# Performance work log

Hardware: AMD Instinct MI355X
Metric: run time of the kernel (lower is better)

## Reference

```python
import jax, jax.numpy as jnp
import numpy as np

D_MODEL = 512
NHEAD = 8
HEAD_DIM = D_MODEL // NHEAD


def setup_inputs() -> dict:
    key = jax.random.key(0)
    ks = jax.random.split(key, 12)
    B, T = 2, 4096
    inp = {
        'query': jax.random.normal(ks[0], (B, T, D_MODEL), jnp.float32),
        'key': jax.random.normal(ks[1], (B, T, D_MODEL), jnp.float32),
        'value': jax.random.normal(ks[2], (B, T, D_MODEL), jnp.float32),
        'frac': jax.random.uniform(ks[3], (B, T), jnp.float32),
        # learned parameters (torch nn.Linear: y = x @ W.T + b)
        'Wq': jax.random.normal(ks[4], (D_MODEL, D_MODEL), jnp.float32) * (D_MODEL ** -0.5),
        'bq': jnp.zeros((D_MODEL,), jnp.float32),
        'Wk': jax.random.normal(ks[5], (D_MODEL, D_MODEL), jnp.float32) * (D_MODEL ** -0.5),
        'bk': jnp.zeros((D_MODEL,), jnp.float32),
        'Wv': jax.random.normal(ks[6], (D_MODEL, D_MODEL), jnp.float32) * (D_MODEL ** -0.5),
        'bv': jnp.zeros((D_MODEL,), jnp.float32),
        'Wo': jax.random.normal(ks[7], (D_MODEL, D_MODEL), jnp.float32) * (D_MODEL ** -0.5),
        'bo': jnp.zeros((D_MODEL,), jnp.float32),
        'alpha_pos': jax.random.normal(ks[8], (NHEAD,), jnp.float32) * 0.1,
        'alpha_neg': jax.random.normal(ks[9], (NHEAD,), jnp.float32) * 0.1,
    }
    return inp


def reference(query, key, value, frac, Wq, bq, Wk, bk, Wv, bv, Wo, bo, alpha_pos, alpha_neg):
    B, T, _ = query.shape
    scale = HEAD_DIM ** -0.5
    # projections (torch Linear convention: x @ W.T + b)
    Q = (query @ Wq.T + bq).reshape(B, T, NHEAD, HEAD_DIM).transpose(0, 2, 1, 3)
    K = (key @ Wk.T + bk).reshape(B, T, NHEAD, HEAD_DIM).transpose(0, 2, 1, 3)
    V = (value @ Wv.T + bv).reshape(B, T, NHEAD, HEAD_DIM).transpose(0, 2, 1, 3)
    scores = jnp.einsum('bhqd,bhkd->bhqk', Q, K) * scale  # [B,H,T,T]
    # stoichiometric bias: D[b,i,j] = frac[b,j] - frac[b,i]
    D = frac[:, None, :] - frac[:, :, None]  # [B,T,T]
    D_pos = jnp.maximum(D, 0.0)
    D_neg = jnp.minimum(D, 0.0)
    bias = (alpha_pos[None, :, None, None] * D_pos[:, None]
            + alpha_neg[None, :, None, None] * D_neg[:, None])  # [B,H,T,T]
    probs = jax.nn.softmax(scores + bias, axis=-1)
    out = jnp.einsum('bhqk,bhkd->bhqd', probs, V)
    out = out.transpose(0, 2, 1, 3).reshape(B, T, D_MODEL)
    return out @ Wo.T + bo
```

## Files before the change

kernel.cpp:

```cpp
#include <hip/hip_runtime.h>

typedef __attribute__((ext_vector_type(8))) __bf16 bf16x8;
typedef __attribute__((ext_vector_type(8))) unsigned short ushort8;
typedef __attribute__((ext_vector_type(4))) unsigned short ushort4_t;
typedef __attribute__((ext_vector_type(4))) float f32x4;
typedef unsigned short ushort_t;

#define MFMA_BF16(A,B,C) __builtin_amdgcn_mfma_f32_16x16x32_bf16(A,B,C,0,0,0)

#define T_SEQ 4096
#define DM 512
#define HD_ 64
#define NH_ 8

#define LOG2E 1.4426950408889634f
#define QSCALE (0.125f * LOG2E)

__device__ __forceinline__ unsigned short f2b(float f){
    unsigned int u = __builtin_bit_cast(unsigned int, f);
    u += 0x7FFFu + ((u >> 16) & 1u);
    return (unsigned short)(u >> 16);
}

__device__ __forceinline__ float exp2_fast(float x){
#if __has_builtin(__builtin_amdgcn_exp2f)
    return __builtin_amdgcn_exp2f(x);
#else
    float r; asm("v_exp_f32 %0, %1" : "=v"(r) : "v"(x)); return r;
#endif
}

__device__ __forceinline__ float max3f(float a, float b, float c){
    return fmaxf(fmaxf(a, b), c);
}

__device__ __forceinline__ unsigned cvt_pk_bf16(float a, float b){
    unsigned r;
    asm("v_cvt_pk_bf16_f32 %0, %1, %2" : "=v"(r) : "v"(a), "v"(b));
    return r;
}

__device__ __forceinline__ void gload_lds16(const void* g, void* l){
    __builtin_amdgcn_global_load_lds((const __attribute__((address_space(1))) void*)g,
                                     (__attribute__((address_space(3))) void*)l, 16, 0, 0);
}

template<int MODE>
__device__ __forceinline__ void gemm_body(const float* __restrict__ A, const float* __restrict__ W,
                                          const float* __restrict__ bias, void* __restrict__ Cout,
                                          int m0, int n0, float scale)
{
    constexpr int K = 512, N = 512;
    __shared__ ushort_t As[128*64];
    __shared__ ushort_t Bs[128*64];

    const int tid  = threadIdx.x;
    const int lane = tid & 63;
    const int w    = tid >> 6;
    const int g    = lane >> 4;
    const int c16  = lane & 15;
    const int wm   = w >> 1, wn = w & 1;

    f32x4 acc[4][4];
#pragma unroll
    for (int i=0;i<4;i++)
#pragma unroll
        for (int j=0;j<4;j++) acc[i][j] = (f32x4){0.f,0.f,0.f,0.f};

#pragma unroll 1
    for (int kt=0; kt<K/64; kt++){
        __syncthreads();
#pragma unroll
        for (int j=0;j<4;j++){
            int cid = j*256 + tid;
            int row = cid >> 3, ch = cid & 7;
            const float* srcA = A + (size_t)(m0+row)*K + kt*64 + ch*8;
            const float* srcB = W + (size_t)(n0+row)*K + kt*64 + ch*8;
            float4 a0 = *(const float4*)srcA;
            float4 a1 = *(const float4*)(srcA+4);
            float4 b0 = *(const float4*)srcB;
            float4 b1 = *(const float4*)(srcB+4);
            ushort8 va, vb;
            va[0]=f2b(a0.x); va[1]=f2b(a0.y); va[2]=f2b(a0.z); va[3]=f2b(a0.w);
            va[4]=f2b(a1.x); va[5]=f2b(a1.y); va[6]=f2b(a1.z); va[7]=f2b(a1.w);
            vb[0]=f2b(b0.x); vb[1]=f2b(b0.y); vb[2]=f2b(b0.z); vb[3]=f2b(b0.w);
            vb[4]=f2b(b1.x); vb[5]=f2b(b1.y); vb[6]=f2b(b1.z); vb[7]=f2b(b1.w);
            int dst = row*64 + ((ch ^ (row & 7))<<3);
            *(ushort8*)&As[dst] = va;
            *(ushort8*)&Bs[dst] = vb;
        }
        __syncthreads();
#pragma unroll
        for (int ks=0; ks<2; ks++){
            bf16x8 af[4], bfr[4];
#pragma unroll
            for (int f=0; f<4; f++){
                int rowa = wm*64 + f*16 + c16;
                af[f]  = *(const bf16x8*)&As[rowa*64 + (((ks*4+g) ^ (rowa&7))<<3)];
                int rowb = wn*64 + f*16 + c16;
                bfr[f] = *(const bf16x8*)&Bs[rowb*64 + (((ks*4+g) ^ (rowb&7))<<3)];
            }
#pragma unroll
            for (int fm=0; fm<4; fm++)
#pragma unroll
                for (int fn=0; fn<4; fn++)
                    acc[fm][fn] = MFMA_BF16(af[fm], bfr[fn], acc[fm][fn]);
        }
    }
#pragma unroll
    for (int fm=0; fm<4; fm++)
#pragma unroll
        for (int fn=0; fn<4; fn++){
            int col = n0 + wn*64 + fn*16 + c16;
            float bv = bias[col];
            if (MODE == 2){
                int t0r = m0 + wm*64 + fm*16 + g*4;
                int b2  = t0r >> 12;
                int t   = t0r & 4095;
                int h2  = col >> 6, d = col & 63;
                ushort4_t u;
#pragma unroll
                for (int r=0; r<4; r++) u[r] = f2b(acc[fm][fn][r] + bv);
                ushort_t* dst = (ushort_t*)Cout + ((size_t)(b2*NH_ + h2)*HD_ + d)*T_SEQ + t;
                *(ushort4_t*)dst = u;
            } else {
#pragma unroll
                for (int r=0; r<4; r++){
                    int rowm = m0 + wm*64 + fm*16 + g*4 + r;
                    float vv = (acc[fm][fn][r] + bv) * scale;
                    if (MODE == 1) ((ushort_t*)Cout)[(size_t)rowm*N + col] = f2b(vv);
                    else           ((float*)Cout)[(size_t)rowm*N + col]   = vv;
                }
            }
        }
}

__global__ __launch_bounds__(256,2) void gemm_qkv_kernel(
    const float* __restrict__ q, const float* __restrict__ k, const float* __restrict__ v,
    const float* __restrict__ Wq, const float* __restrict__ bq,
    const float* __restrict__ Wk, const float* __restrict__ bk,
    const float* __restrict__ Wv, const float* __restrict__ bv,
    ushort_t* __restrict__ QKVp)
{
    int z = blockIdx.z;
    const float* A  = (z==0) ? q  : (z==1 ? k  : v);
    const float* W  = (z==0) ? Wq : (z==1 ? Wk : Wv);
    const float* bb = (z==0) ? bq : (z==1 ? bk : bv);
    ushort_t* C = QKVp + (size_t)z * (size_t)(2*T_SEQ) * DM;
    if (z == 2)
        gemm_body<2>(A, W, bb, C, blockIdx.x*128, blockIdx.y*128, 1.0f);
    else
        gemm_body<1>(A, W, bb, C, blockIdx.x*128, blockIdx.y*128,
                     (z==0) ? QSCALE : 1.0f);
}

__global__ __launch_bounds__(256,2) void gemm_out_kernel(
    const float* __restrict__ O, const float* __restrict__ Wo,
    const float* __restrict__ bo, float* __restrict__ out)
{
    gemm_body<0>(O, Wo, bo, out, blockIdx.x*128, blockIdx.y*128, 1.0f);
}

__global__ __launch_bounds__(512,4) void flash_kernel(
    const ushort_t* __restrict__ Qp, const ushort_t* __restrict__ Kp, const ushort_t* __restrict__ Vt,
    const float* __restrict__ frac, const float* __restrict__ alphap, const float* __restrict__ alphan,
    float* __restrict__ O)
{
    int i    = blockIdx.x;
    int slot = i & 7;
    int seq  = i >> 3;
    int bh   = slot*2 + (seq >> 5);
    int qt   = seq & 31;
    int b    = bh >> 3, h = bh & 7;
    int q0   = qt * 128;

    const int tid  = threadIdx.x;
    const int w    = tid >> 6;
    const int lane = tid & 63;
    const int g    = lane >> 4;
    const int c16  = lane & 15;

    __shared__ ushort_t Ks [2][64*64];
    __shared__ ushort_t VTs[2][64*64];
    __shared__ ushort_t PW [8][16*64];

    const ushort_t* Qbase = Qp + (size_t)(b*T_SEQ)*DM + h*HD_;
    const ushort_t* Kbase = Kp + (size_t)(b*T_SEQ)*DM + h*HD_;
    const ushort_t* Vtb   = Vt + (size_t)bh*HD_*T_SEQ;
    const float*    fr    = frac + b*T_SEQ;
    const float c1 = 0.5f*(alphap[h] + alphan[h]) * LOG2E;
    const float c2 = 0.5f*(alphap[h] - alphan[h]) * LOG2E;
    const int qrow = q0 + w*16;

    bf16x8 qa[2];
#pragma unroll
    for (int ks=0; ks<2; ks++)
        qa[ks] = *(const bf16x8*)(Qbase + (size_t)(qrow + c16)*DM + ks*32 + g*8);
    const float fi = fr[qrow + c16];

    ushort8 ou;
#pragma unroll
    for (int j=0;j<8;j++) ou[j] = 0x3F80;
    const bf16x8 ones = __builtin_bit_cast(bf16x8, ou);

    float m2 = -1e30f;
    f32x4 acc[4];
    f32x4 asum;
#pragma unroll
    for (int dt=0; dt<4; dt++) acc[dt] = (f32x4){0.f,0.f,0.f,0.f};
    asum = (f32x4){0.f,0.f,0.f,0.f};

    bf16x8 vbp[2][4];

#define STAGE(BUF, KV0)                                                          \
    {                                                                            \
        int cb  = w*64;                                                          \
        int idx = cb + lane;                                                     \
        int row = idx >> 3, cc = idx & 7;                                        \
        int cs  = cc ^ (row & 7);                                                \
        gload_lds16(Kbase + (size_t)((KV0)+row)*DM + cs*8, &Ks[BUF][cb*8]);      \
        gload_lds16(Vtb + (size_t)row*T_SEQ + (KV0) + cs*8, &VTs[BUF][cb*8]);    \
    }

    STAGE(0, 0);
    asm volatile("s_waitcnt vmcnt(0)" ::: "memory");
    __syncthreads();

    int buf = 0;
#pragma unroll 1
    for (int kt=0; kt<T_SEQ/64; kt++){
        int kv0 = kt*64;
        if (kt+1 < T_SEQ/64) STAGE(buf^1, kv0+64);

        bf16x8 pb0, pb1;
        if (kt > 0){
            pb0 = *(const bf16x8*)&PW[w][c16*64 + (((    g) ^ (c16&7))<<3)];
            pb1 = *(const bf16x8*)&PW[w][c16*64 + (((4 + g) ^ (c16&7))<<3)];
        }

        f32x4 s[4];
#pragma unroll
        for (int n=0; n<4; n++) s[n] = (f32x4){0.f,0.f,0.f,0.f};
        __builtin_amdgcn_s_setprio(1);
#pragma unroll
        for (int n=0; n<4; n++){
#pragma unroll
            for (int ks=0; ks<2; ks++){
                int row = n*16 + c16;
                bf16x8 kb = *(const bf16x8*)&Ks[buf][row*64 + (((ks*4+g) ^ (row&7))<<3)];
                s[n] = MFMA_BF16(kb, qa[ks], s[n]);
            }
        }
        if (kt > 0){
            asum = MFMA_BF16(ones, pb0, asum);
#pragma unroll
            for (int dt=0; dt<4; dt++) acc[dt] = MFMA_BF16(vbp[0][dt], pb0, acc[dt]);
            asum = MFMA_BF16(ones, pb1, asum);
#pragma unroll
            for (int dt=0; dt<4; dt++) acc[dt] = MFMA_BF16(vbp[1][dt], pb1, acc[dt]);
        }
        __builtin_amdgcn_s_setprio(0);
        __builtin_amdgcn_sched_barrier(0);

#pragma unroll
        for (int n=0; n<4; n++){
            f32x4 fj = *(const f32x4*)&fr[kv0 + n*16 + g*4];
#pragma unroll
            for (int r=0; r<4; r++){
                float dd = fj[r] - fi;
                s[n][r] = fmaf(c1, dd, fmaf(c2, fabsf(dd), s[n][r]));
            }
        }
        float mx;
        {
            float t0 = max3f(s[0][0], s[0][1], s[0][2]);
            float t1 = max3f(s[0][3], s[1][0], s[1][1]);
            float t2 = max3f(s[1][2], s[1][3], s[2][0]);
            float t3 = max3f(s[2][1], s[2][2], s[2][3]);
            float t4 = max3f(s[3][0], s[3][1], s[3][2]);
            mx = fmaxf(max3f(t0, t1, t2), max3f(t3, t4, s[3][3]));
        }
        mx = fmaxf(mx, __shfl_xor(mx, 16));
        mx = fmaxf(mx, __shfl_xor(mx, 32));

        if (__any(mx > m2 + 12.0f)){
            float mnew = fmaxf(m2, mx);
            float fac  = exp2_fast(m2 - mnew);
#pragma unroll
            for (int r=0; r<4; r++) asum[r] *= fac;
#pragma unroll
            for (int dt=0; dt<4; dt++)
#pragma unroll
                for (int r=0; r<4; r++) acc[dt][r] *= fac;
            m2 = mnew;
        }

#pragma unroll
        for (int n=0; n<4; n++){
#pragma unroll
            for (int r=0; r<4; r++) s[n][r] = exp2_fast(s[n][r] - m2);
            unsigned pk0 = cvt_pk_bf16(s[n][0], s[n][1]);
            unsigned pk1 = cvt_pk_bf16(s[n][2], s[n][3]);
            uint2 u; u.x = pk0; u.y = pk1;
            int off = c16*64 + (((n*2 + (g>>1)) ^ (c16 & 7))<<3) + ((g&1)<<2);
            *(uint2*)&PW[w][off] = u;
        }

#pragma unroll
        for (int ks=0; ks<2; ks++)
#pragma unroll
            for (int dt=0; dt<4; dt++){
                int vr = dt*16 + c16;
                vbp[ks][dt] = *(const bf16x8*)&VTs[buf][vr*64 + (((ks*4+g) ^ (vr&7))<<3)];
            }

        asm volatile("s_waitcnt vmcnt(0)" ::: "memory");
        __syncthreads();
        buf ^= 1;
    }
#undef STAGE

    {
        bf16x8 pb0 = *(const bf16x8*)&PW[w][c16*64 + (((    g) ^ (c16&7))<<3)];
        bf16x8 pb1 = *(const bf16x8*)&PW[w][c16*64 + (((4 + g) ^ (c16&7))<<3)];
        asum = MFMA_BF16(ones, pb0, asum);
#pragma unroll
        for (int dt=0; dt<4; dt++) acc[dt] = MFMA_BF16(vbp[0][dt], pb0, acc[dt]);
        asum = MFMA_BF16(ones, pb1, asum);
#pragma unroll
        for (int dt=0; dt<4; dt++) acc[dt] = MFMA_BF16(vbp[1][dt], pb1, acc[dt]);
    }

    float inv = 1.0f / asum[0];
    float* orow = O + (size_t)(b*T_SEQ + qrow + c16)*DM + h*HD_;
#pragma unroll
    for (int dt=0; dt<4; dt++){
        float4 o4;
        o4.x = acc[dt][0]*inv; o4.y = acc[dt][1]*inv;
        o4.z = acc[dt][2]*inv; o4.w = acc[dt][3]*inv;
        *(float4*)(orow + dt*16 + g*4) = o4;
    }
}

extern "C" void kernel_launch(void* const* d_in, const int* in_sizes, int n_in,
                              void* d_out, int out_size, void* d_ws, size_t ws_size,
                              hipStream_t stream)
{
    const float* q  = (const float*)d_in[0];
    const float* k  = (const float*)d_in[1];
    const float* v  = (const float*)d_in[2];
    const float* fr = (const float*)d_in[3];
    const float* Wq = (const float*)d_in[4];
    const float* bq = (const float*)d_in[5];
    const float* Wk = (const float*)d_in[6];
    const float* bk = (const float*)d_in[7];
    const float* Wv = (const float*)d_in[8];
    const float* bv = (const float*)d_in[9];
    const float* Wo = (const float*)d_in[10];
    const float* bo = (const float*)d_in[11];
    const float* ap = (const float*)d_in[12];
    const float* an = (const float*)d_in[13];

    const size_t MT = (size_t)(2*T_SEQ) * DM;
    ushort_t* QKVp = (ushort_t*)d_ws;
    float*    O    = (float*)((char*)d_ws + 3*MT*sizeof(ushort_t));

    dim3 gq(64, 4, 3);
    gemm_qkv_kernel<<<gq, 256, 0, stream>>>(q,k,v,Wq,bq,Wk,bk,Wv,bv,QKVp);

    flash_kernel<<<512, 512, 0, stream>>>(QKVp, QKVp + MT, QKVp + 2*MT, fr, ap, an, O);

    dim3 go(64, 4, 1);
    gemm_out_kernel<<<go, 256, 0, stream>>>(O, Wo, bo, (float*)d_out);
}
```

Measured before the change: 167.0 us.

## Split flash attention over three KV segments and merge partial softmax results

The attention kernel is split-K over the key sequence: each (batch, head, q-tile) is processed by three blocks covering about a third of the KV tiles each. Each block writes unnormalized bf16 partial outputs plus its running max and sum, and a new merge kernel rescales and combines them into fp32 before the output projection. This raises the grid from 512 to 1536 blocks to fill more CUs and hide latency, at the cost of extra partial-output traffic, an extra launch, bf16 rounding of the unnormalized partials, and reuse of the output and workspace buffers as scratch.

```diff
diff --git a/kernel.cpp b/kernel.cpp
--- a/kernel.cpp
+++ b/kernel.cpp
@@ -15,11 +15,17 @@
 
 #define LOG2E 1.4426950408889634f
 #define QSCALE (0.125f * LOG2E)
+#define MT4 ((size_t)4194304)
 
 __device__ __forceinline__ unsigned short f2b(float f){
     unsigned int u = __builtin_bit_cast(unsigned int, f);
     u += 0x7FFFu + ((u >> 16) & 1u);
     return (unsigned short)(u >> 16);
+}
+
+__device__ __forceinline__ float b2f(unsigned short u){
+    unsigned int x = ((unsigned int)u) << 16;
+    return __builtin_bit_cast(float, x);
 }
 
 __device__ __forceinline__ float exp2_fast(float x){
@@ -146,7 +152,7 @@
     const float* A  = (z==0) ? q  : (z==1 ? k  : v);
     const float* W  = (z==0) ? Wq : (z==1 ? Wk : Wv);
     const float* bb = (z==0) ? bq : (z==1 ? bk : bv);
-    ushort_t* C = QKVp + (size_t)z * (size_t)(2*T_SEQ) * DM;
+    ushort_t* C = QKVp + (size_t)z * MT4;
     if (z == 2)
         gemm_body<2>(A, W, bb, C, blockIdx.x*128, blockIdx.y*128, 1.0f);
     else
@@ -164,15 +170,19 @@
 __global__ __launch_bounds__(512,4) void flash_kernel(
     const ushort_t* __restrict__ Qp, const ushort_t* __restrict__ Kp, const ushort_t* __restrict__ Vt,
     const float* __restrict__ frac, const float* __restrict__ alphap, const float* __restrict__ alphan,
-    float* __restrict__ O)
+    ushort_t* __restrict__ Op01, ushort_t* __restrict__ Op2, float2* __restrict__ ml)
 {
     int i    = blockIdx.x;
-    int slot = i & 7;
-    int seq  = i >> 3;
-    int bh   = slot*2 + (seq >> 5);
-    int qt   = seq & 31;
+    int xcd  = i & 7;
+    int j    = i >> 3;
+    int strm = xcd*6 + (j>>5);
+    int qt   = j & 31;
+    int bh   = strm / 3;
+    int seg  = strm - bh*3;
     int b    = bh >> 3, h = bh & 7;
     int q0   = qt * 128;
+    const int kt0 = seg*21;
+    const int nt  = (seg==2) ? 22 : 21;
 
     const int tid  = threadIdx.x;
     const int w    = tid >> 6;
@@ -200,7 +210,7 @@
 
     ushort8 ou;
 #pragma unroll
-    for (int j=0;j<8;j++) ou[j] = 0x3F80;
+    for (int jj=0;jj<8;jj++) ou[jj] = 0x3F80;
     const bf16x8 ones = __builtin_bit_cast(bf16x8, ou);
 
     float m2 = -1e30f;
@@ -222,18 +232,18 @@
         gload_lds16(Vtb + (size_t)row*T_SEQ + (KV0) + cs*8, &VTs[BUF][cb*8]);    \
     }
 
-    STAGE(0, 0);
+    STAGE(0, kt0*64);
     asm volatile("s_waitcnt vmcnt(0)" ::: "memory");
     __syncthreads();
 
     int buf = 0;
 #pragma unroll 1
-    for (int kt=0; kt<T_SEQ/64; kt++){
+    for (int kt=kt0; kt<kt0+nt; kt++){
         int kv0 = kt*64;
-        if (kt+1 < T_SEQ/64) STAGE(buf^1, kv0+64);
+        if (kt+1 < kt0+nt) STAGE(buf^1, kv0+64);
 
         bf16x8 pb0, pb1;
-        if (kt > 0){
+        if (kt > kt0){
             pb0 = *(const bf16x8*)&PW[w][c16*64 + (((    g) ^ (c16&7))<<3)];
             pb1 = *(const bf16x8*)&PW[w][c16*64 + (((4 + g) ^ (c16&7))<<3)];
         }
@@ -251,7 +261,7 @@
                 s[n] = MFMA_BF16(kb, qa[ks], s[n]);
             }
         }
-        if (kt > 0){
+        if (kt > kt0){
             asum = MFMA_BF16(ones, pb0, asum);
 #pragma unroll
             for (int dt=0; dt<4; dt++) acc[dt] = MFMA_BF16(vbp[0][dt], pb0, acc[dt]);
@@ -331,15 +341,55 @@
         for (int dt=0; dt<4; dt++) acc[dt] = MFMA_BF16(vbp[1][dt], pb1, acc[dt]);
     }
 
-    float inv = 1.0f / asum[0];
-    float* orow = O + (size_t)(b*T_SEQ + qrow + c16)*DM + h*HD_;
+    ushort_t* obase = (seg < 2) ? (Op01 + (size_t)seg*MT4) : Op2;
+    ushort_t* orow  = obase + (size_t)(b*T_SEQ + qrow + c16)*DM + h*HD_;
 #pragma unroll
     for (int dt=0; dt<4; dt++){
-        float4 o4;
-        o4.x = acc[dt][0]*inv; o4.y = acc[dt][1]*inv;
-        o4.z = acc[dt][2]*inv; o4.w = acc[dt][3]*inv;
-        *(float4*)(orow + dt*16 + g*4) = o4;
-    }
+        ushort4_t u;
+#pragma unroll
+        for (int r=0; r<4; r++) u[r] = f2b(acc[dt][r]);
+        *(ushort4_t*)(orow + dt*16 + g*4) = u;
+    }
+    if (g == 0){
+        float2 v2; v2.x = m2; v2.y = asum[0];
+        ml[(size_t)(seg*16 + bh)*T_SEQ + (qrow + c16)] = v2;
+    }
+}
+
+__global__ __launch_bounds__(256) void merge3_kernel(const ushort_t* __restrict__ Op01,
+                                                     const ushort_t* __restrict__ Op2,
+                                                     const float2* __restrict__ ml,
+                                                     float* __restrict__ Obf)
+{
+    int idx = blockIdx.x*256 + threadIdx.x;
+    int d8  = idx & 7;
+    int h   = (idx >> 3) & 7;
+    int row = idx >> 6;
+    int b   = row >> 12, t = row & 4095;
+    int bh  = b*NH_ + h;
+
+    float2 p0 = ml[(size_t)bh*T_SEQ + t];
+    float2 p1 = ml[(size_t)(16 + bh)*T_SEQ + t];
+    float2 p2 = ml[(size_t)(32 + bh)*T_SEQ + t];
+    float M  = max3f(p0.x, p1.x, p2.x);
+    float w0 = exp2_fast(p0.x - M);
+    float w1 = exp2_fast(p1.x - M);
+    float w2 = exp2_fast(p2.x - M);
+    float inv = 1.0f / (p0.y*w0 + p1.y*w1 + p2.y*w2);
+    float s0 = w0*inv, s1 = w1*inv, s2 = w2*inv;
+
+    size_t off = (size_t)row*DM + h*HD_ + d8*8;
+    ushort8 a0 = *(const ushort8*)(Op01 + off);
+    ushort8 a1 = *(const ushort8*)(Op01 + MT4 + off);
+    ushort8 a2 = *(const ushort8*)(Op2 + off);
+    float o[8];
+#pragma unroll
+    for (int r=0; r<8; r++)
+        o[r] = b2f(a0[r])*s0 + b2f(a1[r])*s1 + b2f(a2[r])*s2;
+    float4 o0; o0.x=o[0]; o0.y=o[1]; o0.z=o[2]; o0.w=o[3];
+    float4 o1; o1.x=o[4]; o1.y=o[5]; o1.z=o[6]; o1.w=o[7];
+    *(float4*)(Obf + off)     = o0;
+    *(float4*)(Obf + off + 4) = o1;
 }
 
 extern "C" void kernel_launch(void* const* d_in, const int* in_sizes, int n_in,
@@ -361,15 +411,20 @@
     const float* ap = (const float*)d_in[12];
     const float* an = (const float*)d_in[13];
 
-    const size_t MT = (size_t)(2*T_SEQ) * DM;
     ushort_t* QKVp = (ushort_t*)d_ws;
-    float*    O    = (float*)((char*)d_ws + 3*MT*sizeof(ushort_t));
+    ushort_t* Op2  = QKVp + 3*MT4;
+    float2*   mlb  = (float2*)(QKVp + 4*MT4);
+    ushort_t* Op01 = (ushort_t*)d_out;
+    float*    Obf  = (float*)d_ws;
 
     dim3 gq(64, 4, 3);
     gemm_qkv_kernel<<<gq, 256, 0, stream>>>(q,k,v,Wq,bq,Wk,bk,Wv,bv,QKVp);
 
-    flash_kernel<<<512, 512, 0, stream>>>(QKVp, QKVp + MT, QKVp + 2*MT, fr, ap, an, O);
+    flash_kernel<<<1536, 512, 0, stream>>>(QKVp, QKVp + MT4, QKVp + 2*MT4, fr, ap, an,
+                                           Op01, Op2, mlb);
+
+    merge3_kernel<<<2048, 256, 0, stream>>>(Op01, Op2, mlb, Obf);
 
     dim3 go(64, 4, 1);
-    gemm_out_kernel<<<go, 256, 0, stream>>>(O, Wo, bo, (float*)d_out);
-}
+    gemm_out_kernel<<<go, 256, 0, stream>>>(Obf, Wo, bo, (float*)d_out);
+}
```

After: 195.6 us. 1.17x slower.
